# Performance work log

Measured on AMD Instinct MI355X. Metric: run time of the kernel, lower is better.

## Reference

```python
import jax, jax.numpy as jnp
import numpy as np

D_MODEL = 1024
NHEAD = 16
D_HEAD = D_MODEL // NHEAD
D_FF = 2 * D_MODEL
EPS = 1e-5


def setup_inputs() -> dict:
    key = jax.random.key(0)
    ks = jax.random.split(key, 12)
    s = 1.0 / np.sqrt(D_MODEL)
    x = jax.random.normal(ks[0], (4, 1024, D_MODEL), dtype=jnp.float32)
    # per-head projections stacked: [H, d_model, d_head] (x @ W layout)
    wq = jax.random.normal(ks[1], (NHEAD, D_MODEL, D_HEAD), dtype=jnp.float32) * s
    bq = jnp.zeros((NHEAD, D_HEAD), dtype=jnp.float32)
    wk = jax.random.normal(ks[2], (NHEAD, D_MODEL, D_HEAD), dtype=jnp.float32) * s
    bk = jnp.zeros((NHEAD, D_HEAD), dtype=jnp.float32)
    wv = jax.random.normal(ks[3], (NHEAD, D_MODEL, D_HEAD), dtype=jnp.float32) * s
    bv = jnp.zeros((NHEAD, D_HEAD), dtype=jnp.float32)
    wo_w = jax.random.normal(ks[4], (D_MODEL, D_MODEL), dtype=jnp.float32) * s
    wo_b = jnp.zeros((D_MODEL,), dtype=jnp.float32)
    ff1_w = jax.random.normal(ks[5], (D_MODEL, D_FF), dtype=jnp.float32) * s
    ff1_b = jnp.zeros((D_FF,), dtype=jnp.float32)
    ff2_w = jax.random.normal(ks[6], (D_FF, D_MODEL), dtype=jnp.float32) * (1.0 / np.sqrt(D_FF))
    ff2_b = jnp.zeros((D_MODEL,), dtype=jnp.float32)
    g1 = jnp.ones((D_MODEL,), dtype=jnp.float32)
    b1 = jnp.zeros((D_MODEL,), dtype=jnp.float32)
    g2 = jnp.ones((D_MODEL,), dtype=jnp.float32)
    b2 = jnp.zeros((D_MODEL,), dtype=jnp.float32)
    return dict(x=x, wq=wq, bq=bq, wk=wk, bk=bk, wv=wv, bv=bv,
                wo_w=wo_w, wo_b=wo_b, g1=g1, b1=b1,
                ff1_w=ff1_w, ff1_b=ff1_b, ff2_w=ff2_w, ff2_b=ff2_b,
                g2=g2, b2=b2)


def manual_layernorm(x, gamma, beta):
    # faithful to source: (x - mean) / (std + eps), std unbiased=False
    mean = jnp.mean(x, axis=-1, keepdims=True)
    std = jnp.sqrt(jnp.mean((x - mean) ** 2, axis=-1, keepdims=True))
    return gamma * (x - mean) / (std + EPS) + beta


def reference(x, wq, bq, wk, bk, wv, bv, wo_w, wo_b, g1, b1,
              ff1_w, ff1_b, ff2_w, ff2_b, g2, b2):
    B, S, D = x.shape
    # per-head projections, vectorized over heads: [B,H,S,d_head]
    q = jnp.einsum('bsd,hdk->bhsk', x, wq) + bq[None, :, None, :]
    k = jnp.einsum('bsd,hdk->bhsk', x, wk) + bk[None, :, None, :]
    v = jnp.einsum('bsd,hdk->bhsk', x, wv) + bv[None, :, None, :]
    scores = jnp.einsum('bhsk,bhtk->bhst', q, k) / jnp.sqrt(jnp.float32(D_HEAD))
    weights = jax.nn.softmax(scores, axis=-1)
    attn = jnp.einsum('bhst,bhtk->bhsk', weights, v)
    # concat heads back to [B,S,D]
    concat = jnp.transpose(attn, (0, 2, 1, 3)).reshape(B, S, D)
    proj = concat @ wo_w + wo_b
    h = manual_layernorm(x + proj, g1, b1)
    ff = jax.nn.relu(h @ ff1_w + ff1_b) @ ff2_w + ff2_b
    return manual_layernorm(h + ff, g2, b2)
```

## Files before the change

kernel.cpp:

```cpp
#include <hip/hip_runtime.h>
#include <hip/hip_bf16.h>

typedef __attribute__((ext_vector_type(8))) short bf16x8;
typedef __attribute__((ext_vector_type(4))) float f32x4;
using bf16 = __hip_bfloat16;

#define NTOK 4096
#define EPS_LN 1e-5f
#define QSCL 0.1803368801111244f

enum { EPI_F32 = 0, EPI_QKV = 1, EPI_RELU_BF16 = 2 };

#define VM8 asm volatile("s_waitcnt vmcnt(8)" ::: "memory")
#define VM0 asm volatile("s_waitcnt vmcnt(0)" ::: "memory")
#define LGKM0 asm volatile("s_waitcnt lgkmcnt(0)" ::: "memory")
#define SCHED0 __builtin_amdgcn_sched_barrier(0)
#define NOVM
#define DSRO(dst, ad, off) \
  asm volatile("ds_read_b128 %0, %1 offset:" #off : "=v"(dst) : "v"(ad))

__device__ inline void gload_lds16(const void* g, void* l) {
  __builtin_amdgcn_global_load_lds(
      (const __attribute__((address_space(1))) char*)g,
      (__attribute__((address_space(3))) char*)l, 16, 0, 0);
}

__device__ inline unsigned ldsoff(const void* p) {
  return (unsigned)(size_t)(const __attribute__((address_space(3))) char*)p;
}

__device__ inline unsigned short f2bfu(float x) {
  bf16 h = __float2bfloat16(x);
  return __builtin_bit_cast(unsigned short, h);
}
__device__ inline bf16 to_bf16(float v) { return __float2bfloat16(v); }
__device__ inline bf16 to_bf16(bf16 v) { return v; }


__global__ __launch_bounds__(256) void cvt_bf16_kernel(const float* __restrict__ src,
                                                       bf16* __restrict__ dst, int n4) {
  int i = blockIdx.x * 256 + threadIdx.x;
  if (i >= n4) return;
  float4 v = ((const float4*)src)[i];
  ushort4 o;
  o.x = f2bfu(v.x); o.y = f2bfu(v.y); o.z = f2bfu(v.z); o.w = f2bfu(v.w);
  ((ushort4*)dst)[i] = o;
}

template <typename ST>
__global__ __launch_bounds__(256) void transpose_cvt(const ST* __restrict__ src,
                                                     bf16* __restrict__ dst, int R, int C) {
  __shared__ bf16 tile[32][33];
  int o = blockIdx.z;
  int r0 = blockIdx.y * 32, c0 = blockIdx.x * 32;
  int tx = threadIdx.x & 31, ty = threadIdx.x >> 5;
  const ST* s = src + (size_t)o * R * C;
  bf16* d = dst + (size_t)o * R * C;
#pragma unroll
  for (int i = 0; i < 32; i += 8)
    tile[ty + i][tx] = to_bf16(s[(size_t)(r0 + ty + i) * C + (c0 + tx)]);
  __syncthreads();
#pragma unroll
  for (int i = 0; i < 32; i += 8)
    d[(size_t)(c0 + ty + i) * R + (r0 + tx)] = tile[tx][ty + i];
}

__global__ __launch_bounds__(256) void pack_bias_kernel(const float* __restrict__ bq,
                                                        const float* __restrict__ bk,
                                                        const float* __restrict__ bv,
                                                        float* __restrict__ out) {
  int i = blockIdx.x * 256 + threadIdx.x;
  if (i >= 3072) return;
  out[i] = (i < 1024) ? bq[i] : (i < 2048 ? bk[i - 1024] : bv[i - 2048]);
}


#define STG(KOFF, DD) { _Pragma("unroll") for (int q = 0; q < 4; ++q) { \
    gload_lds16(gA0 + (KOFF) + (size_t)(q * 32) * lda2, \
                sAb + (DD) * 16384 + q * 4096 + w * 1024); \
    gload_lds16(gB0 + (KOFF) + (size_t)(q * 32) * ldb2, \
                sBb + (DD) * 16384 + q * 4096 + w * 1024); } }

#define TILE(OFFLIT, STG_, VMS) { \
  _Pragma("unroll") for (int i = 0; i < 4; ++i) { \
    DSRO(a[i][0], adA[i][0], OFFLIT); \
    DSRO(a[i][1], adA[i][1], OFFLIT); \
  } \
  _Pragma("unroll") for (int j = 0; j < 4; ++j) { \
    DSRO(b[j][0], adB[j][0], OFFLIT); \
    DSRO(b[j][1], adB[j][1], OFFLIT); \
  } \
  LGKM0; SCHED0; \
  __builtin_amdgcn_s_barrier(); \
  STG_; \
  __builtin_amdgcn_s_setprio(1); \
  _Pragma("unroll") for (int i = 0; i < 4; ++i) \
  _Pragma("unroll") for (int j = 0; j < 4; ++j) \
  _Pragma("unroll") for (int kk = 0; kk < 2; ++kk) \
    acc[i][j] = __builtin_amdgcn_mfma_f32_16x16x32_bf16( \
        a[i][kk], b[j][kk], acc[i][j], 0, 0, 0); \
  __builtin_amdgcn_s_setprio(0); \
  VMS; \
  __builtin_amdgcn_s_barrier(); }

__global__ __launch_bounds__(256, 2) void gemm128(
    const bf16* __restrict__ A, int lda,
    const bf16* __restrict__ Bt, int ldb,
    int M, int N, int K,
    int nbm, int nbn,
    const float* __restrict__ bias,
    float* __restrict__ Cf, bf16* __restrict__ Cb,
    bf16* __restrict__ Qd, bf16* __restrict__ Kd, bf16* __restrict__ Vd,
    int mode) {
  __shared__ bf16 sA[2][128][64];
  __shared__ bf16 sB[2][128][64];
  const int nwg = nbm * nbn;
  const int orig = blockIdx.x;
  const int wgid = (orig % 8) * (nwg / 8) + orig / 8;
  const int bm = wgid / nbn, bn = wgid % nbn;
  const int tid = threadIdx.x;
  const int w = tid >> 6, lane = tid & 63;
  const int wm = w >> 1, wn = w & 1;
  const int ri = lane & 15, kg = lane >> 4;
  const bf16* Ab = A + (size_t)bm * 128 * lda;
  const bf16* Bb = Bt + (size_t)bn * 128 * ldb;
  const int NT = K / 64;
  const size_t lda2 = (size_t)lda * 2, ldb2 = (size_t)ldb * 2;
  char* sAb = (char*)&sA[0][0][0];
  char* sBb = (char*)&sB[0][0][0];

  unsigned adA[4][2], adB[4][2];
  const unsigned sA0 = ldsoff(sAb), sB0 = ldsoff(sBb);
#pragma unroll
  for (int i = 0; i < 4; ++i) {
    int row = wm * 64 + i * 16 + ri;
    unsigned swz = (unsigned)((row & 7) << 4);
    adA[i][0] = sA0 + row * 128 + ((kg * 16) ^ swz);
    adA[i][1] = sA0 + row * 128 + ((64 + kg * 16) ^ swz);
  }
#pragma unroll
  for (int j = 0; j < 4; ++j) {
    int row = wn * 64 + j * 16 + ri;
    unsigned swz = (unsigned)((row & 7) << 4);
    adB[j][0] = sB0 + row * 128 + ((kg * 16) ^ swz);
    adB[j][1] = sB0 + row * 128 + ((64 + kg * 16) ^ swz);
  }

  const int r0 = tid >> 3;
  const int cb0 = ((tid & 7) * 16) ^ ((r0 & 7) << 4);
  const char* gA0 = (const char*)Ab + (size_t)r0 * lda2 + cb0;
  const char* gB0 = (const char*)Bb + (size_t)r0 * ldb2 + cb0;

  f32x4 acc[4][4] = {};
  bf16x8 a[4][2], b[4][2];

  STG(0, 0) STG(128, 1)
  VM8;
  __builtin_amdgcn_s_barrier();

  const int niter = NT / 2 - 1;
  for (int it = 0; it < niter; ++it) {
    TILE(0,     STG(256, 0), VM8)
    TILE(16384, STG(384, 1), VM8)
    gA0 += 256; gB0 += 256;
  }
  TILE(0,     , VM0)
  TILE(16384, , NOVM)

  const int colbase = bn * 128 + wn * 64 + ri;
  float bv4[4];
#pragma unroll
  for (int nf = 0; nf < 4; ++nf)
    bv4[nf] = bias ? bias[colbase + nf * 16] : 0.f;

  if (mode == EPI_QKV) {
    int col0 = bn * 128 + wn * 64;
    int which = col0 >> 10, hh = (col0 >> 6) & 15;
    bf16* dst = (which == 0) ? Qd : (which == 1) ? Kd : Vd;
    float scl = (which == 0) ? QSCL : 1.0f;
#pragma unroll
    for (int mf = 0; mf < 4; ++mf)
#pragma unroll
      for (int r = 0; r < 4; ++r) {
        int row = bm * 128 + wm * 64 + mf * 16 + kg * 4 + r;
        int b2 = row >> 10, s = row & 1023;
        bf16* o = dst + (((size_t)(b2 * 16 + hh)) * 1024 + s) * 64;
#pragma unroll
        for (int nf = 0; nf < 4; ++nf)
          o[nf * 16 + ri] = __float2bfloat16((acc[mf][nf][r] + bv4[nf]) * scl);
      }
  } else if (mode == EPI_F32) {
#pragma unroll
    for (int mf = 0; mf < 4; ++mf)
#pragma unroll
      for (int r = 0; r < 4; ++r) {
        int row = bm * 128 + wm * 64 + mf * 16 + kg * 4 + r;
        float* o = Cf + (size_t)row * N + colbase;
#pragma unroll
        for (int nf = 0; nf < 4; ++nf) o[nf * 16] = acc[mf][nf][r] + bv4[nf];
      }
  } else {
#pragma unroll
    for (int mf = 0; mf < 4; ++mf)
#pragma unroll
      for (int r = 0; r < 4; ++r) {
        int row = bm * 128 + wm * 64 + mf * 16 + kg * 4 + r;
        bf16* o = Cb + (size_t)row * N + colbase;
#pragma unroll
        for (int nf = 0; nf < 4; ++nf) {
          float v = acc[mf][nf][r] + bv4[nf];
          o[nf * 16] = __float2bfloat16(v > 0.f ? v : 0.f);
        }
      }
  }
}

__global__ __launch_bounds__(256, 4) void attn_kernel(
    const bf16* __restrict__ Qb, const bf16* __restrict__ Kb,
    const bf16* __restrict__ Vs, bf16* __restrict__ Ob) {
  __shared__ bf16 KV[2][2][64][64];
  __shared__ bf16 Ps[4][16][64];
  const int orig = blockIdx.x;
  const int blk = (orig & 7) * 128 + (orig >> 3);
  const int bh = blk >> 4, qt = blk & 15;
  const int bb = bh >> 4, hh = bh & 15;
  const int tid = threadIdx.x, w = tid >> 6, lane = tid & 63;
  const int ri = lane & 15, kg = lane >> 4, r8 = lane >> 3;
  const int cb = ((lane & 7) * 16) ^ ((r8 & 7) << 4);
  const unsigned rsw = (unsigned)((ri & 7) << 4);
  const bf16* qp = Qb + (size_t)bh * 65536;
  const bf16* kp = Kb + (size_t)bh * 65536;
  const bf16* vp = Vs + (size_t)bh * 65536;
  const int q0 = qt * 64 + w * 16;
  const int c0 = w * 2, c1 = c0 + 1;

  unsigned offk0 = (unsigned)((kg * 16) ^ (int)rsw);
  unsigned offk1 = (unsigned)((64 + kg * 16) ^ (int)rsw);
  unsigned adF[4][2];
  const unsigned kv0 = ldsoff(&KV[0][0][0][0]);
#pragma unroll
  for (int n = 0; n < 4; ++n) {
    unsigned row = (unsigned)((n * 16 + ri) * 128);
    adF[n][0] = kv0 + row + offk0;
    adF[n][1] = kv0 + row + offk1;
  }
  const unsigned ps0 = ldsoff(&Ps[0][0][0]) + (unsigned)(w * 2048 + ri * 128);
  unsigned adPr[2] = {ps0 + offk0, ps0 + offk1};
  char* pwb = (char*)&Ps[0][0][0] + w * 2048 + ri * 128;

  bf16x8 qf[2];
  qf[0] = *(const bf16x8*)(qp + (size_t)(q0 + ri) * 64 + kg * 8);
  qf[1] = *(const bf16x8*)(qp + (size_t)(q0 + ri) * 64 + 32 + kg * 8);

  bf16x8 ones;
#pragma unroll
  for (int e = 0; e < 8; ++e) ones[e] = (short)0x3F80;

  f32x4 oacc[4] = {};
  f32x4 lacc = {};
  float mrun = -1e30f;

#define ASTAGE(T, D) { \
    gload_lds16((const char*)(kp + (size_t)((T) * 64 + c0 * 8 + r8) * 64) + cb, \
                (char*)KV + (D) * 16384 + c0 * 1024); \
    gload_lds16((const char*)(kp + (size_t)((T) * 64 + c1 * 8 + r8) * 64) + cb, \
                (char*)KV + (D) * 16384 + c1 * 1024); \
    gload_lds16((const char*)(vp + (size_t)(c0 * 8 + r8) * 1024 + (T) * 64) + cb, \
                (char*)KV + (D) * 16384 + 8192 + c0 * 1024); \
    gload_lds16((const char*)(vp + (size_t)(c1 * 8 + r8) * 1024 + (T) * 64) + cb, \
                (char*)KV + (D) * 16384 + 8192 + c1 * 1024); }

  ASTAGE(0, 0);
  VM0;
  __syncthreads();

  for (int t = 0; t < 16; ++t) {
    const int cur = t & 1;
    if (t < 15) ASTAGE(t + 1, cur ^ 1);
    const unsigned bo = (unsigned)(cur * 16384);

    bf16x8 kf[2][4];
#pragma unroll
    for (int n = 0; n < 4; ++n) {
      DSRO(kf[0][n], adF[n][0] + bo, 0);
      DSRO(kf[1][n], adF[n][1] + bo, 0);
    }
    LGKM0; SCHED0;
    f32x4 sac[4] = {};
#pragma unroll
    for (int n = 0; n < 4; ++n) {
      sac[n] = __builtin_amdgcn_mfma_f32_16x16x32_bf16(kf[0][n], qf[0], sac[n], 0, 0, 0);
      sac[n] = __builtin_amdgcn_mfma_f32_16x16x32_bf16(kf[1][n], qf[1], sac[n], 0, 0, 0);
    }

    float mx[4];
#pragma unroll
    for (int n = 0; n < 4; ++n)
      mx[n] = fmaxf(fmaxf(sac[n][0], sac[n][1]), fmaxf(sac[n][2], sac[n][3]));
    float mt16 = fmaxf(fmaxf(mx[0], mx[1]), fmaxf(mx[2], mx[3]));
    if (!__all(mt16 - mrun <= 8.f)) {
      float mrow = fmaxf(mt16, __shfl_xor(mt16, 16));
      mrow = fmaxf(mrow, __shfl_xor(mrow, 32));
      float mnew = fmaxf(mrun, mrow);
      float corr = exp2f(mrun - mnew);
      mrun = mnew;
      float cr[4];
#pragma unroll
      for (int r = 0; r < 4; ++r) cr[r] = __shfl(corr, kg * 4 + r);
#pragma unroll
      for (int n = 0; n < 4; ++n) {
        oacc[n][0] *= cr[0]; oacc[n][1] *= cr[1];
        oacc[n][2] *= cr[2]; oacc[n][3] *= cr[3];
      }
      lacc[0] *= cr[0]; lacc[1] *= cr[1]; lacc[2] *= cr[2]; lacc[3] *= cr[3];
    }
#pragma unroll
    for (int n = 0; n < 4; ++n) {
      float p0 = exp2f(sac[n][0] - mrun);
      float p1 = exp2f(sac[n][1] - mrun);
      float p2 = exp2f(sac[n][2] - mrun);
      float p3 = exp2f(sac[n][3] - mrun);
      ushort4 pk;
      pk.x = f2bfu(p0); pk.y = f2bfu(p1);
      pk.z = f2bfu(p2); pk.w = f2bfu(p3);
      *(ushort4*)(pwb + (((n * 32 + kg * 8)) ^ (int)rsw)) = pk;
    }
    LGKM0;

    bf16x8 pf[2], vf[2][4];
    DSRO(pf[0], adPr[0], 0);
    DSRO(pf[1], adPr[1], 0);
#pragma unroll
    for (int n = 0; n < 4; ++n) {
      DSRO(vf[0][n], adF[n][0] + bo, 8192);
      DSRO(vf[1][n], adF[n][1] + bo, 8192);
    }
    LGKM0; SCHED0;
#pragma unroll
    for (int n = 0; n < 4; ++n) {
      oacc[n] = __builtin_amdgcn_mfma_f32_16x16x32_bf16(pf[0], vf[0][n], oacc[n], 0, 0, 0);
      oacc[n] = __builtin_amdgcn_mfma_f32_16x16x32_bf16(pf[1], vf[1][n], oacc[n], 0, 0, 0);
    }
    lacc = __builtin_amdgcn_mfma_f32_16x16x32_bf16(pf[0], ones, lacc, 0, 0, 0);
    lacc = __builtin_amdgcn_mfma_f32_16x16x32_bf16(pf[1], ones, lacc, 0, 0, 0);
    if (t < 15) {
      VM0;
      __syncthreads();
    }
  }

  float ivr[4];
#pragma unroll
  for (int r = 0; r < 4; ++r) ivr[r] = 1.f / lacc[r];
#pragma unroll
  for (int r = 0; r < 4; ++r) {
    int s = q0 + kg * 4 + r;
    size_t base = ((size_t)(bb * 1024 + s)) * 1024 + hh * 64;
#pragma unroll
    for (int n = 0; n < 4; ++n)
      Ob[base + n * 16 + ri] = __float2bfloat16(oacc[n][r] * ivr[r]);
  }
#undef ASTAGE
}

__global__ __launch_bounds__(256) void ln_kernel(
    const float* __restrict__ a, const float* __restrict__ b,
    const float* __restrict__ gamma, const float* __restrict__ beta,
    float* __restrict__ out_f32, bf16* __restrict__ out_bf16) {
  int row = blockIdx.x;
  int tid = threadIdx.x;
  float4 av = ((const float4*)(a + (size_t)row * 1024))[tid];
  float4 bv = ((const float4*)(b + (size_t)row * 1024))[tid];
  float4 z;
  z.x = av.x + bv.x; z.y = av.y + bv.y; z.z = av.z + bv.z; z.w = av.w + bv.w;
  float s = z.x + z.y + z.z + z.w;
  float ss = z.x * z.x + z.y * z.y + z.z * z.z + z.w * z.w;
#pragma unroll
  for (int o = 32; o >= 1; o >>= 1) { s += __shfl_xor(s, o); ss += __shfl_xor(ss, o); }
  __shared__ float red[8];
  int wid = tid >> 6;
  if ((tid & 63) == 0) { red[wid] = s; red[4 + wid] = ss; }
  __syncthreads();
  s = red[0] + red[1] + red[2] + red[3];
  ss = red[4] + red[5] + red[6] + red[7];
  float mean = s * (1.f / 1024.f);
  float var = ss * (1.f / 1024.f) - mean * mean;
  var = var > 0.f ? var : 0.f;
  float inv = 1.f / (sqrtf(var) + EPS_LN);
  float4 g = ((const float4*)gamma)[tid];
  float4 be = ((const float4*)beta)[tid];
  float4 y;
  y.x = (z.x - mean) * inv * g.x + be.x;
  y.y = (z.y - mean) * inv * g.y + be.y;
  y.z = (z.z - mean) * inv * g.z + be.z;
  y.w = (z.w - mean) * inv * g.w + be.w;
  ((float4*)(out_f32 + (size_t)row * 1024))[tid] = y;
  if (out_bf16) {
    ushort4 o;
    o.x = f2bfu(y.x); o.y = f2bfu(y.y); o.z = f2bfu(y.z); o.w = f2bfu(y.w);
    ((ushort4*)(out_bf16 + (size_t)row * 1024))[tid] = o;
  }
}

extern "C" void kernel_launch(void* const* d_in, const int* in_sizes, int n_in,
                              void* d_out, int out_size, void* d_ws, size_t ws_size,
                              hipStream_t stream) {
  const float* x = (const float*)d_in[0];
  const float* wq = (const float*)d_in[1];
  const float* bq = (const float*)d_in[2];
  const float* wk = (const float*)d_in[3];
  const float* bk = (const float*)d_in[4];
  const float* wv = (const float*)d_in[5];
  const float* bv = (const float*)d_in[6];
  const float* wo_w = (const float*)d_in[7];
  const float* wo_b = (const float*)d_in[8];
  const float* g1 = (const float*)d_in[9];
  const float* b1 = (const float*)d_in[10];
  const float* ff1w = (const float*)d_in[11];
  const float* ff1b = (const float*)d_in[12];
  const float* ff2w = (const float*)d_in[13];
  const float* ff2b = (const float*)d_in[14];
  const float* g2 = (const float*)d_in[15];
  const float* b2 = (const float*)d_in[16];

  char* ws = (char*)d_ws;
  size_t off = 0;
  auto alloc = [&](size_t bytes) {
    char* p = ws + off;
    off += (bytes + 255) & ~(size_t)255;
    return p;
  };
  bf16* xb = (bf16*)alloc((size_t)NTOK * 1024 * 2);
  bf16* wqkvt = (bf16*)alloc((size_t)3072 * 1024 * 2);
  bf16* wot = (bf16*)alloc((size_t)1024 * 1024 * 2);
  bf16* ff1t = (bf16*)alloc((size_t)2048 * 1024 * 2);
  bf16* ff2t = (bf16*)alloc((size_t)1024 * 2048 * 2);
  float* qkvbias = (float*)alloc(3072 * 4);
  bf16* qbuf = (bf16*)alloc((size_t)64 * 1024 * 64 * 2);
  bf16* kbuf = (bf16*)alloc((size_t)64 * 1024 * 64 * 2);
  bf16* vbuf = (bf16*)alloc((size_t)64 * 1024 * 64 * 2);
  bf16* vtb = (bf16*)alloc((size_t)64 * 64 * 1024 * 2);
  bf16* attnb = (bf16*)alloc((size_t)NTOK * 1024 * 2);
  float* proj = (float*)alloc((size_t)NTOK * 1024 * 4);
  bf16* hb = (bf16*)alloc((size_t)NTOK * 1024 * 2);
  bf16* ff1o = qbuf;
  float* hbuf = (float*)d_out;

  cvt_bf16_kernel<<<(NTOK * 1024 / 4 + 255) / 256, 256, 0, stream>>>(x, xb, NTOK * 1024 / 4);
  transpose_cvt<float><<<dim3(2, 32, 16), 256, 0, stream>>>(wq, wqkvt, 1024, 64);
  transpose_cvt<float><<<dim3(2, 32, 16), 256, 0, stream>>>(wk, wqkvt + 1024 * 1024, 1024, 64);
  transpose_cvt<float><<<dim3(2, 32, 16), 256, 0, stream>>>(wv, wqkvt + 2 * 1024 * 1024, 1024, 64);
  transpose_cvt<float><<<dim3(32, 32, 1), 256, 0, stream>>>(wo_w, wot, 1024, 1024);
  transpose_cvt<float><<<dim3(64, 32, 1), 256, 0, stream>>>(ff1w, ff1t, 1024, 2048);
  transpose_cvt<float><<<dim3(32, 64, 1), 256, 0, stream>>>(ff2w, ff2t, 2048, 1024);
  pack_bias_kernel<<<12, 256, 0, stream>>>(bq, bk, bv, qkvbias);

  gemm128<<<768, 256, 0, stream>>>(xb, 1024, wqkvt, 1024, 4096, 3072, 1024,
                                   32, 24, qkvbias,
                                   nullptr, nullptr, qbuf, kbuf, vbuf, EPI_QKV);
  transpose_cvt<bf16><<<dim3(2, 32, 64), 256, 0, stream>>>(vbuf, vtb, 1024, 64);
  attn_kernel<<<dim3(1024), 256, 0, stream>>>(qbuf, kbuf, vtb, attnb);
  gemm128<<<256, 256, 0, stream>>>(attnb, 1024, wot, 1024, 4096, 1024, 1024,
                                   32, 8, wo_b,
                                   proj, nullptr, nullptr, nullptr, nullptr, EPI_F32);
  ln_kernel<<<4096, 256, 0, stream>>>(x, proj, g1, b1, hbuf, hb);
  gemm128<<<512, 256, 0, stream>>>(hb, 1024, ff1t, 1024, 4096, 2048, 1024,
                                   32, 16, ff1b,
                                   nullptr, ff1o, nullptr, nullptr, nullptr, EPI_RELU_BF16);
  gemm128<<<256, 256, 0, stream>>>(ff1o, 2048, ff2t, 2048, 4096, 1024, 2048,
                                   32, 8, ff2b,
                                   proj, nullptr, nullptr, nullptr, nullptr, EPI_F32);
  ln_kernel<<<4096, 256, 0, stream>>>(hbuf, proj, g2, b2, (float*)d_out, nullptr);
}
```

Measured before the change: 175.3 us.

## Store GEMM outputs in bf16, read bf16 residual in LN, unroll attention double-buffer

Result: faster. 167.3 us (-4.5%).

```diff
diff --git a/kernel.cpp b/kernel.cpp
--- a/kernel.cpp
+++ b/kernel.cpp
@@ -9,7 +9,7 @@
 #define EPS_LN 1e-5f
 #define QSCL 0.1803368801111244f
 
-enum { EPI_F32 = 0, EPI_QKV = 1, EPI_RELU_BF16 = 2 };
+enum { EPI_F32 = 0, EPI_QKV = 1, EPI_RELU_BF16 = 2, EPI_BF16 = 3 };
 
 #define VM8 asm volatile("s_waitcnt vmcnt(8)" ::: "memory")
 #define VM0 asm volatile("s_waitcnt vmcnt(0)" ::: "memory")
@@ -35,6 +35,16 @@
 }
 __device__ inline bf16 to_bf16(float v) { return __float2bfloat16(v); }
 __device__ inline bf16 to_bf16(bf16 v) { return v; }
+
+__device__ inline unsigned cvtpk(float lo, float hi) {
+  unsigned r;
+  asm volatile("v_cvt_pk_bf16_f32 %0, %1, %2" : "=v"(r) : "v"(lo), "v"(hi));
+  return r;
+}
+__device__ inline float bu2f(unsigned short u) {
+  unsigned v = (unsigned)u << 16;
+  return __builtin_bit_cast(float, v);
+}
 
 
 __global__ __launch_bounds__(256) void cvt_bf16_kernel(const float* __restrict__ src,
@@ -199,7 +209,7 @@
 #pragma unroll
         for (int nf = 0; nf < 4; ++nf) o[nf * 16] = acc[mf][nf][r] + bv4[nf];
       }
-  } else {
+  } else if (mode == EPI_RELU_BF16) {
 #pragma unroll
     for (int mf = 0; mf < 4; ++mf)
 #pragma unroll
@@ -211,6 +221,17 @@
           float v = acc[mf][nf][r] + bv4[nf];
           o[nf * 16] = __float2bfloat16(v > 0.f ? v : 0.f);
         }
+      }
+  } else {
+#pragma unroll
+    for (int mf = 0; mf < 4; ++mf)
+#pragma unroll
+      for (int r = 0; r < 4; ++r) {
+        int row = bm * 128 + wm * 64 + mf * 16 + kg * 4 + r;
+        bf16* o = Cb + (size_t)row * N + colbase;
+#pragma unroll
+        for (int nf = 0; nf < 4; ++nf)
+          o[nf * 16] = __float2bfloat16(acc[mf][nf][r] + bv4[nf]);
       }
   }
 }
@@ -247,6 +268,10 @@
   const unsigned ps0 = ldsoff(&Ps[0][0][0]) + (unsigned)(w * 2048 + ri * 128);
   unsigned adPr[2] = {ps0 + offk0, ps0 + offk1};
   char* pwb = (char*)&Ps[0][0][0] + w * 2048 + ri * 128;
+  char* adPw[4];
+#pragma unroll
+  for (int n = 0; n < 4; ++n)
+    adPw[n] = pwb + ((n * 32 + kg * 8) ^ (int)rsw);
 
   bf16x8 qf[2];
   qf[0] = *(const bf16x8*)(qp + (size_t)(q0 + ri) * 64 + kg * 8);
@@ -270,84 +295,73 @@
     gload_lds16((const char*)(vp + (size_t)(c1 * 8 + r8) * 1024 + (T) * 64) + cb, \
                 (char*)KV + (D) * 16384 + 8192 + c1 * 1024); }
 
+#define ATILE(KOFF, VOFF, STG_, ENDSYNC) { \
+  bf16x8 kf0[4], kf1[4]; \
+  _Pragma("unroll") for (int n = 0; n < 4; ++n) { \
+    DSRO(kf0[n], adF[n][0], KOFF); \
+    DSRO(kf1[n], adF[n][1], KOFF); \
+  } \
+  STG_; \
+  LGKM0; SCHED0; \
+  f32x4 sac[4] = {}; \
+  _Pragma("unroll") for (int n = 0; n < 4; ++n) { \
+    sac[n] = __builtin_amdgcn_mfma_f32_16x16x32_bf16(kf0[n], qf[0], sac[n], 0, 0, 0); \
+    sac[n] = __builtin_amdgcn_mfma_f32_16x16x32_bf16(kf1[n], qf[1], sac[n], 0, 0, 0); \
+  } \
+  float mx[4]; \
+  _Pragma("unroll") for (int n = 0; n < 4; ++n) \
+    mx[n] = fmaxf(fmaxf(sac[n][0], sac[n][1]), fmaxf(sac[n][2], sac[n][3])); \
+  float mt16 = fmaxf(fmaxf(mx[0], mx[1]), fmaxf(mx[2], mx[3])); \
+  if (!__all(mt16 - mrun <= 8.f)) { \
+    float mrow = fmaxf(mt16, __shfl_xor(mt16, 16)); \
+    mrow = fmaxf(mrow, __shfl_xor(mrow, 32)); \
+    float mnew = fmaxf(mrun, mrow); \
+    float corr = exp2f(mrun - mnew); \
+    mrun = mnew; \
+    float cr[4]; \
+    _Pragma("unroll") for (int r = 0; r < 4; ++r) cr[r] = __shfl(corr, kg * 4 + r); \
+    _Pragma("unroll") for (int n = 0; n < 4; ++n) { \
+      oacc[n][0] *= cr[0]; oacc[n][1] *= cr[1]; \
+      oacc[n][2] *= cr[2]; oacc[n][3] *= cr[3]; \
+    } \
+    lacc[0] *= cr[0]; lacc[1] *= cr[1]; lacc[2] *= cr[2]; lacc[3] *= cr[3]; \
+  } \
+  _Pragma("unroll") for (int n = 0; n < 4; ++n) { \
+    uint2 pk; \
+    pk.x = cvtpk(exp2f(sac[n][0] - mrun), exp2f(sac[n][1] - mrun)); \
+    pk.y = cvtpk(exp2f(sac[n][2] - mrun), exp2f(sac[n][3] - mrun)); \
+    *(uint2*)adPw[n] = pk; \
+  } \
+  LGKM0; \
+  bf16x8 pf0, pf1, vf0[4], vf1[4]; \
+  DSRO(pf0, adPr[0], 0); \
+  DSRO(pf1, adPr[1], 0); \
+  _Pragma("unroll") for (int n = 0; n < 4; ++n) { \
+    DSRO(vf0[n], adF[n][0], VOFF); \
+    DSRO(vf1[n], adF[n][1], VOFF); \
+  } \
+  LGKM0; SCHED0; \
+  _Pragma("unroll") for (int n = 0; n < 4; ++n) { \
+    oacc[n] = __builtin_amdgcn_mfma_f32_16x16x32_bf16(pf0, vf0[n], oacc[n], 0, 0, 0); \
+    oacc[n] = __builtin_amdgcn_mfma_f32_16x16x32_bf16(pf1, vf1[n], oacc[n], 0, 0, 0); \
+  } \
+  lacc = __builtin_amdgcn_mfma_f32_16x16x32_bf16(pf0, ones, lacc, 0, 0, 0); \
+  lacc = __builtin_amdgcn_mfma_f32_16x16x32_bf16(pf1, ones, lacc, 0, 0, 0); \
+  ENDSYNC }
+
+#define SYNCT { VM0; __syncthreads(); }
+
   ASTAGE(0, 0);
   VM0;
   __syncthreads();
 
-  for (int t = 0; t < 16; ++t) {
-    const int cur = t & 1;
-    if (t < 15) ASTAGE(t + 1, cur ^ 1);
-    const unsigned bo = (unsigned)(cur * 16384);
-
-    bf16x8 kf[2][4];
-#pragma unroll
-    for (int n = 0; n < 4; ++n) {
-      DSRO(kf[0][n], adF[n][0] + bo, 0);
-      DSRO(kf[1][n], adF[n][1] + bo, 0);
-    }
-    LGKM0; SCHED0;
-    f32x4 sac[4] = {};
-#pragma unroll
-    for (int n = 0; n < 4; ++n) {
-      sac[n] = __builtin_amdgcn_mfma_f32_16x16x32_bf16(kf[0][n], qf[0], sac[n], 0, 0, 0);
-      sac[n] = __builtin_amdgcn_mfma_f32_16x16x32_bf16(kf[1][n], qf[1], sac[n], 0, 0, 0);
-    }
-
-    float mx[4];
-#pragma unroll
-    for (int n = 0; n < 4; ++n)
-      mx[n] = fmaxf(fmaxf(sac[n][0], sac[n][1]), fmaxf(sac[n][2], sac[n][3]));
-    float mt16 = fmaxf(fmaxf(mx[0], mx[1]), fmaxf(mx[2], mx[3]));
-    if (!__all(mt16 - mrun <= 8.f)) {
-      float mrow = fmaxf(mt16, __shfl_xor(mt16, 16));
-      mrow = fmaxf(mrow, __shfl_xor(mrow, 32));
-      float mnew = fmaxf(mrun, mrow);
-      float corr = exp2f(mrun - mnew);
-      mrun = mnew;
-      float cr[4];
-#pragma unroll
-      for (int r = 0; r < 4; ++r) cr[r] = __shfl(corr, kg * 4 + r);
-#pragma unroll
-      for (int n = 0; n < 4; ++n) {
-        oacc[n][0] *= cr[0]; oacc[n][1] *= cr[1];
-        oacc[n][2] *= cr[2]; oacc[n][3] *= cr[3];
-      }
-      lacc[0] *= cr[0]; lacc[1] *= cr[1]; lacc[2] *= cr[2]; lacc[3] *= cr[3];
-    }
-#pragma unroll
-    for (int n = 0; n < 4; ++n) {
-      float p0 = exp2f(sac[n][0] - mrun);
-      float p1 = exp2f(sac[n][1] - mrun);
-      float p2 = exp2f(sac[n][2] - mrun);
-      float p3 = exp2f(sac[n][3] - mrun);
-      ushort4 pk;
-      pk.x = f2bfu(p0); pk.y = f2bfu(p1);
-      pk.z = f2bfu(p2); pk.w = f2bfu(p3);
-      *(ushort4*)(pwb + (((n * 32 + kg * 8)) ^ (int)rsw)) = pk;
-    }
-    LGKM0;
-
-    bf16x8 pf[2], vf[2][4];
-    DSRO(pf[0], adPr[0], 0);
-    DSRO(pf[1], adPr[1], 0);
-#pragma unroll
-    for (int n = 0; n < 4; ++n) {
-      DSRO(vf[0][n], adF[n][0] + bo, 8192);
-      DSRO(vf[1][n], adF[n][1] + bo, 8192);
-    }
-    LGKM0; SCHED0;
-#pragma unroll
-    for (int n = 0; n < 4; ++n) {
-      oacc[n] = __builtin_amdgcn_mfma_f32_16x16x32_bf16(pf[0], vf[0][n], oacc[n], 0, 0, 0);
-      oacc[n] = __builtin_amdgcn_mfma_f32_16x16x32_bf16(pf[1], vf[1][n], oacc[n], 0, 0, 0);
-    }
-    lacc = __builtin_amdgcn_mfma_f32_16x16x32_bf16(pf[0], ones, lacc, 0, 0, 0);
-    lacc = __builtin_amdgcn_mfma_f32_16x16x32_bf16(pf[1], ones, lacc, 0, 0, 0);
-    if (t < 15) {
-      VM0;
-      __syncthreads();
-    }
-  }
+  for (int tt = 0; tt < 7; ++tt) {
+    const int t2 = tt * 2;
+    ATILE(0,     8192,  ASTAGE(t2 + 1, 1), SYNCT)
+    ATILE(16384, 24576, ASTAGE(t2 + 2, 0), SYNCT)
+  }
+  ATILE(0,     8192,  ASTAGE(15, 1), SYNCT)
+  ATILE(16384, 24576, ,              )
 
   float ivr[4];
 #pragma unroll
@@ -361,18 +375,23 @@
       Ob[base + n * 16 + ri] = __float2bfloat16(oacc[n][r] * ivr[r]);
   }
 #undef ASTAGE
-}
-
-__global__ __launch_bounds__(256) void ln_kernel(
-    const float* __restrict__ a, const float* __restrict__ b,
+#undef ATILE
+#undef SYNCT
+}
+
+__global__ __launch_bounds__(256) void ln_bb(
+    const bf16* __restrict__ a, const bf16* __restrict__ b,
     const float* __restrict__ gamma, const float* __restrict__ beta,
     float* __restrict__ out_f32, bf16* __restrict__ out_bf16) {
   int row = blockIdx.x;
   int tid = threadIdx.x;
-  float4 av = ((const float4*)(a + (size_t)row * 1024))[tid];
-  float4 bv = ((const float4*)(b + (size_t)row * 1024))[tid];
+  ushort4 au = ((const ushort4*)(a + (size_t)row * 1024))[tid];
+  ushort4 bu = ((const ushort4*)(b + (size_t)row * 1024))[tid];
   float4 z;
-  z.x = av.x + bv.x; z.y = av.y + bv.y; z.z = av.z + bv.z; z.w = av.w + bv.w;
+  z.x = bu2f(au.x) + bu2f(bu.x);
+  z.y = bu2f(au.y) + bu2f(bu.y);
+  z.z = bu2f(au.z) + bu2f(bu.z);
+  z.w = bu2f(au.w) + bu2f(bu.w);
   float s = z.x + z.y + z.z + z.w;
   float ss = z.x * z.x + z.y * z.y + z.z * z.z + z.w * z.w;
 #pragma unroll
@@ -395,11 +414,46 @@
   y.z = (z.z - mean) * inv * g.z + be.z;
   y.w = (z.w - mean) * inv * g.w + be.w;
   ((float4*)(out_f32 + (size_t)row * 1024))[tid] = y;
-  if (out_bf16) {
-    ushort4 o;
-    o.x = f2bfu(y.x); o.y = f2bfu(y.y); o.z = f2bfu(y.z); o.w = f2bfu(y.w);
-    ((ushort4*)(out_bf16 + (size_t)row * 1024))[tid] = o;
-  }
+  ushort4 o;
+  o.x = f2bfu(y.x); o.y = f2bfu(y.y); o.z = f2bfu(y.z); o.w = f2bfu(y.w);
+  ((ushort4*)(out_bf16 + (size_t)row * 1024))[tid] = o;
+}
+
+__global__ __launch_bounds__(256) void ln_fb(
+    const float* __restrict__ a, const bf16* __restrict__ b,
+    const float* __restrict__ gamma, const float* __restrict__ beta,
+    float* __restrict__ out_f32) {
+  int row = blockIdx.x;
+  int tid = threadIdx.x;
+  float4 av = ((const float4*)(a + (size_t)row * 1024))[tid];
+  ushort4 bu = ((const ushort4*)(b + (size_t)row * 1024))[tid];
+  float4 z;
+  z.x = av.x + bu2f(bu.x);
+  z.y = av.y + bu2f(bu.y);
+  z.z = av.z + bu2f(bu.z);
+  z.w = av.w + bu2f(bu.w);
+  float s = z.x + z.y + z.z + z.w;
+  float ss = z.x * z.x + z.y * z.y + z.z * z.z + z.w * z.w;
+#pragma unroll
+  for (int o = 32; o >= 1; o >>= 1) { s += __shfl_xor(s, o); ss += __shfl_xor(ss, o); }
+  __shared__ float red[8];
+  int wid = tid >> 6;
+  if ((tid & 63) == 0) { red[wid] = s; red[4 + wid] = ss; }
+  __syncthreads();
+  s = red[0] + red[1] + red[2] + red[3];
+  ss = red[4] + red[5] + red[6] + red[7];
+  float mean = s * (1.f / 1024.f);
+  float var = ss * (1.f / 1024.f) - mean * mean;
+  var = var > 0.f ? var : 0.f;
+  float inv = 1.f / (sqrtf(var) + EPS_LN);
+  float4 g = ((const float4*)gamma)[tid];
+  float4 be = ((const float4*)beta)[tid];
+  float4 y;
+  y.x = (z.x - mean) * inv * g.x + be.x;
+  y.y = (z.y - mean) * inv * g.y + be.y;
+  y.z = (z.z - mean) * inv * g.z + be.z;
+  y.w = (z.w - mean) * inv * g.w + be.w;
+  ((float4*)(out_f32 + (size_t)row * 1024))[tid] = y;
 }
 
 extern "C" void kernel_launch(void* const* d_in, const int* in_sizes, int n_in,
@@ -441,7 +495,7 @@
   bf16* vbuf = (bf16*)alloc((size_t)64 * 1024 * 64 * 2);
   bf16* vtb = (bf16*)alloc((size_t)64 * 64 * 1024 * 2);
   bf16* attnb = (bf16*)alloc((size_t)NTOK * 1024 * 2);
-  float* proj = (float*)alloc((size_t)NTOK * 1024 * 4);
+  bf16* projb = (bf16*)alloc((size_t)NTOK * 1024 * 2);
   bf16* hb = (bf16*)alloc((size_t)NTOK * 1024 * 2);
   bf16* ff1o = qbuf;
   float* hbuf = (float*)d_out;
@@ -462,13 +516,13 @@
   attn_kernel<<<dim3(1024), 256, 0, stream>>>(qbuf, kbuf, vtb, attnb);
   gemm128<<<256, 256, 0, stream>>>(attnb, 1024, wot, 1024, 4096, 1024, 1024,
                                    32, 8, wo_b,
-                                   proj, nullptr, nullptr, nullptr, nullptr, EPI_F32);
-  ln_kernel<<<4096, 256, 0, stream>>>(x, proj, g1, b1, hbuf, hb);
+                                   nullptr, projb, nullptr, nullptr, nullptr, EPI_BF16);
+  ln_bb<<<4096, 256, 0, stream>>>(xb, projb, g1, b1, hbuf, hb);
   gemm128<<<512, 256, 0, stream>>>(hb, 1024, ff1t, 1024, 4096, 2048, 1024,
                                    32, 16, ff1b,
                                    nullptr, ff1o, nullptr, nullptr, nullptr, EPI_RELU_BF16);
   gemm128<<<256, 256, 0, stream>>>(ff1o, 2048, ff2t, 2048, 4096, 1024, 2048,
                                    32, 8, ff2b,
-                                   proj, nullptr, nullptr, nullptr, nullptr, EPI_F32);
-  ln_kernel<<<4096, 256, 0, stream>>>(hbuf, proj, g2, b2, (float*)d_out, nullptr);
-}
+                                   nullptr, projb, nullptr, nullptr, nullptr, EPI_BF16);
+  ln_fb<<<4096, 256, 0, stream>>>(hbuf, projb, g2, b2, (float*)d_out);
+}
```
